# Kernel optimization log

Hardware: AMD Instinct MI355X
Metric: run time of the kernel (lower is better)

## Reference

```python
import jax, jax.numpy as jnp
import numpy as np

N = 8192      # num nodes
E = 262144    # num edges (avg degree 32)
IN = 512
HID = 512
LAT = 128


def setup_inputs() -> dict:
    key = jax.random.key(0)
    ks = jax.random.split(key, 8)
    edge_index = jax.random.randint(ks[0], (2, E), 0, N, dtype=jnp.int64 if jax.config.read('jax_enable_x64') else jnp.int32)
    x = jax.random.normal(ks[1], (N, IN), jnp.float32)
    def w(k, i, o):
        return jax.random.normal(k, (i, o), jnp.float32) * (1.0 / np.sqrt(i))
    return {
        'edge_index': edge_index,
        'x': x,
        'W1': w(ks[2], IN, HID), 'b1': jnp.zeros((HID,), jnp.float32),
        'Wmu': w(ks[3], HID, LAT), 'bmu': jnp.zeros((LAT,), jnp.float32),
        'Wlv': w(ks[4], HID, LAT), 'blv': jnp.zeros((LAT,), jnp.float32),
    }


def gcn_conv(x, row, col, W, b):
    # PyG GCNConv: h = x W; symmetric norm with self-loops (added by caller);
    # out[i] = sum_{(j->i)} d_j^{-1/2} d_i^{-1/2} h[j] + b
    h = x @ W
    ones = jnp.ones((row.shape[0],), h.dtype)
    deg = jax.ops.segment_sum(ones, col, num_segments=N)  # in-degree incl. self-loop
    dinv_sqrt = jnp.where(deg > 0, jax.lax.rsqrt(jnp.maximum(deg, 1e-12)), 0.0)
    norm = dinv_sqrt[row] * dinv_sqrt[col]                # [E+N]
    out = jax.ops.segment_sum(norm[:, None] * h[row], col, num_segments=N)
    return out + b


def reference(edge_index, x, W1, b1, Wmu, bmu, Wlv, blv):
    # add self-loops once, reuse for all layers
    loops = jnp.arange(N, dtype=edge_index.dtype)
    row = jnp.concatenate([edge_index[0], loops])
    col = jnp.concatenate([edge_index[1], loops])

    h = jax.nn.relu(gcn_conv(x, row, col, W1, b1))
    mu = gcn_conv(h, row, col, Wmu, bmu)
    logvar = gcn_conv(h, row, col, Wlv, blv)
    z = mu  # eval-mode reparameterize (deterministic)
    A_pred = jax.nn.sigmoid(z @ z.T)  # [N, N] dot-product decode
    return (A_pred, mu, logvar, z)
```

## Files before the change

kernel.cpp:

```cpp
#include <hip/hip_runtime.h>
#include <math.h>

#define NNODES 8192
#define NEDGES 262144
#define FIN 512
#define FHID 512
#define FLAT 128

typedef unsigned short bfu;
typedef __attribute__((ext_vector_type(8))) short short8;
typedef __attribute__((ext_vector_type(4))) float f32x4;
typedef __attribute__((ext_vector_type(2))) float f32x2;
typedef __attribute__((ext_vector_type(4))) unsigned short us4;

__device__ __forceinline__ float bf2f(unsigned short u) {
    union { unsigned int i; float f; } c; c.i = ((unsigned int)u) << 16; return c.f;
}
__device__ __forceinline__ unsigned short f2bf(float f) {
    union { float f; unsigned int i; } c; c.f = f;
    unsigned int i = c.i;
    unsigned int r = (i + 0x7FFFu + ((i >> 16) & 1u)) >> 16;
    return (unsigned short)r;
}

__global__ void k_zero(int* p, int n) {
    int i = blockIdx.x * blockDim.x + threadIdx.x;
    if (i < n) p[i] = 0;
}

__global__ void k_count(const int* __restrict__ ei, int* __restrict__ deg) {
    int e = blockIdx.x * blockDim.x + threadIdx.x;
    if (e < NEDGES) atomicAdd(&deg[ei[NEDGES + e]], 1);
}

__global__ void k_scan(const int* __restrict__ deg, int* __restrict__ row_start,
                       float* __restrict__ dinv) {
    __shared__ int part[256];
    int t = threadIdx.x, base = t * 32;
    int s = 0;
    for (int i = 0; i < 32; i++) s += deg[base + i];
    part[t] = s;
    __syncthreads();
    for (int off = 1; off < 256; off <<= 1) {
        int v = (t >= off) ? part[t - off] : 0;
        __syncthreads();
        part[t] += v;
        __syncthreads();
    }
    int run = (t == 0) ? 0 : part[t - 1];
    for (int i = 0; i < 32; i++) {
        int d = deg[base + i];
        row_start[base + i] = run;
        run += d;
        dinv[base + i] = rsqrtf((float)(d + 1));
    }
    if (t == 255) row_start[NNODES] = run;
}

__global__ void k_scatter(const int* __restrict__ ei, const int* __restrict__ row_start,
                          int* __restrict__ cursor, int* __restrict__ csr,
                          const float* __restrict__ dinv, float* __restrict__ wcsr) {
    int e = blockIdx.x * blockDim.x + threadIdx.x;
    if (e < NEDGES) {
        int src = ei[e];
        int dst = ei[NEDGES + e];
        int p = atomicAdd(&cursor[dst], 1);
        int pos = row_start[dst] + p;
        csr[pos] = src;
        wcsr[pos] = dinv[src];
    }
}

__global__ void k_prep_const(const float* __restrict__ W1, const float* __restrict__ Wmu,
                             const float* __restrict__ Wlv, const float* __restrict__ x,
                             bfu* __restrict__ Bt1, bfu* __restrict__ Bt2,
                             bfu* __restrict__ xb) {
    __shared__ bfu tile[32][33];
    int b = blockIdx.x;
    if (b < 256) {
        int tx = threadIdx.x & 31, ty = threadIdx.x >> 5;
        int nb = b & 15, kb = b >> 4;
        int n0 = nb * 32, k0 = kb * 32;
#pragma unroll
        for (int i = 0; i < 32; i += 8)
            tile[ty + i][tx] = f2bf(W1[(size_t)(k0 + ty + i) * 512 + n0 + tx]);
        __syncthreads();
#pragma unroll
        for (int i = 0; i < 32; i += 8)
            Bt1[(size_t)(n0 + ty + i) * 512 + k0 + tx] = tile[tx][ty + i];
    } else if (b < 384) {
        int bb = b - 256;
        int tx = threadIdx.x & 31, ty = threadIdx.x >> 5;
        int nb = bb & 7, kb = bb >> 3;
        int n0 = nb * 32, k0 = kb * 32;
        const float* Wsel = (n0 < 128) ? Wmu : Wlv;
        int noff = (n0 < 128) ? 0 : 128;
#pragma unroll
        for (int i = 0; i < 32; i += 8)
            tile[ty + i][tx] = f2bf(Wsel[(size_t)(k0 + ty + i) * 128 + (n0 + tx - noff)]);
        __syncthreads();
#pragma unroll
        for (int i = 0; i < 32; i += 8)
            Bt2[(size_t)(n0 + ty + i) * 512 + k0 + tx] = tile[tx][ty + i];
    } else {
        int i = (b - 384) * 256 + threadIdx.x;
        const float4 v = ((const float4*)x)[i];
        ushort2 lo = {f2bf(v.x), f2bf(v.y)};
        ushort2 hi = {f2bf(v.z), f2bf(v.w)};
        ((ushort2*)xb)[2 * i] = lo;
        ((ushort2*)xb)[2 * i + 1] = hi;
    }
}

template <int TM, int TN>
__global__ void k_gemm_nt(const bfu* __restrict__ A, const bfu* __restrict__ Bt,
                          bfu* __restrict__ C, int M, int N, int K) {
    int wid  = (blockIdx.x * blockDim.x + threadIdx.x) >> 6;
    int lane = threadIdx.x & 63;
    int l = lane & 15, q = lane >> 4;
    int tn = N / (16 * TN);
    int m0 = (wid / tn) * (16 * TM), n0 = (wid % tn) * (16 * TN);

    f32x4 acc[TM][TN];
#pragma unroll
    for (int a = 0; a < TM; a++)
#pragma unroll
        for (int b = 0; b < TN; b++) acc[a][b] = (f32x4){0.f, 0.f, 0.f, 0.f};

    const bfu* Ap = A + (size_t)(m0 + l) * K + q * 8;
    const bfu* Bp = Bt + (size_t)(n0 + l) * K + q * 8;

    for (int k0 = 0; k0 < K; k0 += 32) {
        short8 av[TM], bv[TN];
#pragma unroll
        for (int mi = 0; mi < TM; mi++)
            av[mi] = *(const short8*)(Ap + (size_t)mi * 16 * K + k0);
#pragma unroll
        for (int ni = 0; ni < TN; ni++)
            bv[ni] = *(const short8*)(Bp + (size_t)ni * 16 * K + k0);
#pragma unroll
        for (int mi = 0; mi < TM; mi++)
#pragma unroll
            for (int ni = 0; ni < TN; ni++)
                acc[mi][ni] = __builtin_amdgcn_mfma_f32_16x16x32_bf16(bv[ni], av[mi],
                                                                     acc[mi][ni], 0, 0, 0);
    }

#pragma unroll
    for (int mi = 0; mi < TM; mi++) {
        int row = m0 + mi * 16 + l;
#pragma unroll
        for (int ni = 0; ni < TN; ni++) {
            int col = n0 + ni * 16 + q * 4;
            f32x4 v = acc[mi][ni];
            us4 o = {f2bf(v[0]), f2bf(v[1]), f2bf(v[2]), f2bf(v[3])};
            *(us4*)(C + (size_t)row * N + col) = o;
        }
    }
}

__global__ __launch_bounds__(256) void k_decode_sym(const bfu* __restrict__ Z,
                                                    float* __restrict__ C) {
    __shared__ float ldsT[4][2][16][68];
    int wid  = (blockIdx.x * blockDim.x + threadIdx.x) >> 6;
    int wv   = threadIdx.x >> 6;
    int lane = threadIdx.x & 63;
    int l = lane & 15, q = lane >> 4;

    int idx = wid;
    int ti = (int)((257.0 - sqrt(66049.0 - 8.0 * (double)idx)) * 0.5);
    if (ti > 127) ti = 127;
    if (ti < 0) ti = 0;
    while (ti > 0 && (ti * (257 - ti)) / 2 > idx) ti--;
    while (ti < 127 && ((ti + 1) * (256 - ti)) / 2 <= idx) ti++;
    int tj = ti + (idx - (ti * (257 - ti)) / 2);
    int m0 = ti * 64, n0 = tj * 64;

    f32x4 acc[4][4];
#pragma unroll
    for (int a = 0; a < 4; a++)
#pragma unroll
        for (int b = 0; b < 4; b++) acc[a][b] = (f32x4){0.f, 0.f, 0.f, 0.f};

    const bfu* Ap = Z + (size_t)(m0 + l) * 128 + q * 8;
    const bfu* Bp = Z + (size_t)(n0 + l) * 128 + q * 8;

#pragma unroll
    for (int k0 = 0; k0 < 128; k0 += 32) {
        short8 av[4], bv[4];
#pragma unroll
        for (int mi = 0; mi < 4; mi++)
            av[mi] = *(const short8*)(Ap + (size_t)mi * 16 * 128 + k0);
#pragma unroll
        for (int ni = 0; ni < 4; ni++)
            bv[ni] = *(const short8*)(Bp + (size_t)ni * 16 * 128 + k0);
#pragma unroll
        for (int mi = 0; mi < 4; mi++)
#pragma unroll
            for (int ni = 0; ni < 4; ni++)
                acc[mi][ni] = __builtin_amdgcn_mfma_f32_16x16x32_bf16(bv[ni], av[mi],
                                                                     acc[mi][ni], 0, 0, 0);
    }

#pragma unroll
    for (int mi = 0; mi < 4; mi++)
#pragma unroll
        for (int ni = 0; ni < 4; ni++)
#pragma unroll
            for (int r = 0; r < 4; r++)
                acc[mi][ni][r] = __builtin_amdgcn_rcpf(1.0f + __expf(-acc[mi][ni][r]));

#pragma unroll
    for (int mi = 0; mi < 4; mi++) {
        int row = m0 + mi * 16 + l;
#pragma unroll
        for (int ni = 0; ni < 4; ni++) {
            int col = n0 + ni * 16 + q * 4;
            __builtin_nontemporal_store(acc[mi][ni], (f32x4*)(C + (size_t)row * 8192 + col));
        }
    }

    if (ti != tj) {
#pragma unroll
        for (int ni = 0; ni < 4; ni++) {
            int p = ni & 1;
#pragma unroll
            for (int mi = 0; mi < 4; mi++)
#pragma unroll
                for (int r = 0; r < 4; r++)
                    ldsT[wv][p][q * 4 + r][mi * 16 + l] = acc[mi][ni][r];
            asm volatile("s_waitcnt lgkmcnt(0)" ::: "memory");
#pragma unroll
            for (int j = 0; j < 16; j++) {
                float v = ldsT[wv][p][j][lane];
                __builtin_nontemporal_store(
                    v, C + (size_t)(n0 + ni * 16 + j) * 8192 + m0 + lane);
            }
        }
    }
}

template <int F>
__device__ __forceinline__ void agg_core(const bfu* __restrict__ hin,
                                         const int* __restrict__ csr,
                                         const float* __restrict__ wcsr,
                                         int s, int e, int i, int f, float di,
                                         float& a0, float& a1) {
    a0 = 0.f; a1 = 0.f;
    int ed = s;
    for (; ed + 4 <= e; ed += 4) {
        int s0 = csr[ed], s1 = csr[ed + 1], s2 = csr[ed + 2], s3 = csr[ed + 3];
        float w0 = wcsr[ed], w1 = wcsr[ed + 1], w2 = wcsr[ed + 2], w3 = wcsr[ed + 3];
        unsigned int p0 = *(const unsigned int*)(hin + (size_t)s0 * F + f);
        unsigned int p1 = *(const unsigned int*)(hin + (size_t)s1 * F + f);
        unsigned int p2 = *(const unsigned int*)(hin + (size_t)s2 * F + f);
        unsigned int p3 = *(const unsigned int*)(hin + (size_t)s3 * F + f);
        a0 += w0 * bf2f((unsigned short)(p0 & 0xFFFF));
        a1 += w0 * bf2f((unsigned short)(p0 >> 16));
        a0 += w1 * bf2f((unsigned short)(p1 & 0xFFFF));
        a1 += w1 * bf2f((unsigned short)(p1 >> 16));
        a0 += w2 * bf2f((unsigned short)(p2 & 0xFFFF));
        a1 += w2 * bf2f((unsigned short)(p2 >> 16));
        a0 += w3 * bf2f((unsigned short)(p3 & 0xFFFF));
        a1 += w3 * bf2f((unsigned short)(p3 >> 16));
    }
    for (; ed < e; ed++) {
        int src = csr[ed];
        float w = wcsr[ed];
        unsigned int pk = *(const unsigned int*)(hin + (size_t)src * F + f);
        a0 += w * bf2f((unsigned short)(pk & 0xFFFF));
        a1 += w * bf2f((unsigned short)(pk >> 16));
    }
    unsigned int pk = *(const unsigned int*)(hin + (size_t)i * F + f);
    a0 += di * bf2f((unsigned short)(pk & 0xFFFF));
    a1 += di * bf2f((unsigned short)(pk >> 16));
}

__global__ void k_agg1(const bfu* __restrict__ hin, const int* __restrict__ csr,
                       const float* __restrict__ wcsr, const int* __restrict__ rs,
                       const float* __restrict__ dinv, const float* __restrict__ bias,
                       bfu* __restrict__ hout) {
    int i = blockIdx.x;
    int f = threadIdx.x * 2;
    float di = dinv[i];
    float a0, a1;
    agg_core<FHID>(hin, csr, wcsr, rs[i], rs[i + 1], i, f, di, a0, a1);
    float o0 = fmaxf(di * a0 + bias[f], 0.f);
    float o1 = fmaxf(di * a1 + bias[f + 1], 0.f);
    unsigned int outw = (unsigned int)f2bf(o0) | ((unsigned int)f2bf(o1) << 16);
    *(unsigned int*)(hout + (size_t)i * FHID + f) = outw;
}

__global__ void k_agg2(const bfu* __restrict__ hin, const int* __restrict__ csr,
                       const float* __restrict__ wcsr, const int* __restrict__ rs,
                       const float* __restrict__ dinv, const float* __restrict__ bmu,
                       const float* __restrict__ blv, float* __restrict__ out_mu,
                       float* __restrict__ out_lv, float* __restrict__ out_z,
                       bfu* __restrict__ ws_z) {
    int i = blockIdx.x;
    int f = threadIdx.x * 2;
    float di = dinv[i];
    float a0, a1;
    agg_core<256>(hin, csr, wcsr, rs[i], rs[i + 1], i, f, di, a0, a1);
    float v0 = di * a0, v1 = di * a1;
    if (f < 128) {
        v0 += bmu[f]; v1 += bmu[f + 1];
        f32x2 fv = {v0, v1};
        __builtin_nontemporal_store(fv, (f32x2*)(out_mu + (size_t)i * FLAT + f));
        __builtin_nontemporal_store(fv, (f32x2*)(out_z + (size_t)i * FLAT + f));
        unsigned int bw = (unsigned int)f2bf(v0) | ((unsigned int)f2bf(v1) << 16);
        *(unsigned int*)(ws_z + (size_t)i * FLAT + f) = bw;
    } else {
        int fl = f - 128;
        v0 += blv[fl]; v1 += blv[fl + 1];
        f32x2 fv = {v0, v1};
        __builtin_nontemporal_store(fv, (f32x2*)(out_lv + (size_t)i * FLAT + fl));
    }
}

extern "C" void kernel_launch(void* const* d_in, const int* in_sizes, int n_in,
                              void* d_out, int out_size, void* d_ws, size_t ws_size,
                              hipStream_t stream) {
    const int*   ei  = (const int*)d_in[0];
    const float* x   = (const float*)d_in[1];
    const float* W1  = (const float*)d_in[2];
    const float* b1  = (const float*)d_in[3];
    const float* Wmu = (const float*)d_in[4];
    const float* bmu = (const float*)d_in[5];
    const float* Wlv = (const float*)d_in[6];
    const float* blv = (const float*)d_in[7];
    float* out = (float*)d_out;

    char* wsb = (char*)d_ws;
    size_t off = 0;
    auto alloc = [&](size_t bytes) -> char* {
        char* p = wsb + off;
        off += (bytes + 255) & ~(size_t)255;
        return p;
    };
    int*   deg       = (int*)alloc(NNODES * 4);
    int*   cursor    = (int*)alloc(NNODES * 4);
    int*   row_start = (int*)alloc((NNODES + 1) * 4);
    float* dinv      = (float*)alloc(NNODES * 4);
    int*   csr       = (int*)alloc(NEDGES * 4);
    float* wcsr      = (float*)alloc(NEDGES * 4);
    bfu*   Bt1       = (bfu*)alloc(512 * 512 * 2);
    bfu*   Bt2       = (bfu*)alloc(256 * 512 * 2);
    bfu*   xb        = (bfu*)alloc((size_t)NNODES * FIN * 2);
    bfu*   h0        = (bfu*)alloc((size_t)NNODES * FHID * 2);
    bfu*   h         = (bfu*)alloc((size_t)NNODES * FHID * 2);
    bfu*   hml       = (bfu*)alloc((size_t)NNODES * 256 * 2);
    bfu*   zb        = (bfu*)alloc((size_t)NNODES * FLAT * 2);

    float* out_mu = out + (size_t)NNODES * NNODES;
    float* out_lv = out_mu + (size_t)NNODES * FLAT;
    float* out_z  = out_lv + (size_t)NNODES * FLAT;

    k_zero<<<(2 * NNODES + 255) / 256, 256, 0, stream>>>(deg, 2 * NNODES);
    k_count<<<NEDGES / 256, 256, 0, stream>>>(ei, deg);
    k_scan<<<1, 256, 0, stream>>>(deg, row_start, dinv);
    k_scatter<<<NEDGES / 256, 256, 0, stream>>>(ei, row_start, cursor, csr, dinv, wcsr);
    k_prep_const<<<256 + 128 + 4096, 256, 0, stream>>>(W1, Wmu, Wlv, x, Bt1, Bt2, xb);

    k_gemm_nt<4, 2><<<(8192 / 64) * (512 / 32) / 4, 256, 0, stream>>>(
        xb, Bt1, h0, 8192, 512, 512);
    k_agg1<<<NNODES, 256, 0, stream>>>(h0, csr, wcsr, row_start, dinv, b1, h);

    k_gemm_nt<2, 2><<<(8192 / 32) * (256 / 32) / 4, 256, 0, stream>>>(
        h, Bt2, hml, 8192, 256, 512);
    k_agg2<<<NNODES, 128, 0, stream>>>(hml, csr, wcsr, row_start, dinv, bmu, blv,
                                       out_mu, out_lv, out_z, zb);

    k_decode_sym<<<8256 / 4, 256, 0, stream>>>(zb, out);
}
```

Before: 450.9 us.

## Vectorize GCN aggregation per wavefront, pack edge pairs, merge prep kernels

Aggregation kernels now assign one wavefront per node, and each lane loads 8 (or 4) bf16 features as a single wide vector. Neighbour index and weight are packed into one int2 array so each edge needs a single load. The CSR scatter is merged with the weight/x preparation kernel to save a launch. The decode transpose store now writes 16-byte vectors instead of scalars. Together these aim to cut memory instruction count and launch overhead, at the cost of more registers per lane and fewer independent edges in flight per lane.

Measured after the change: 448.6 us. About the same (-0.5%).

```diff
diff --git a/kernel.cpp b/kernel.cpp
--- a/kernel.cpp
+++ b/kernel.cpp
@@ -21,6 +21,23 @@
     unsigned int i = c.i;
     unsigned int r = (i + 0x7FFFu + ((i >> 16) & 1u)) >> 16;
     return (unsigned short)r;
+}
+
+__device__ __forceinline__ void acc8(float* acc, uint4 v, float w) {
+    acc[0] += w * bf2f((unsigned short)(v.x & 0xFFFF));
+    acc[1] += w * bf2f((unsigned short)(v.x >> 16));
+    acc[2] += w * bf2f((unsigned short)(v.y & 0xFFFF));
+    acc[3] += w * bf2f((unsigned short)(v.y >> 16));
+    acc[4] += w * bf2f((unsigned short)(v.z & 0xFFFF));
+    acc[5] += w * bf2f((unsigned short)(v.z >> 16));
+    acc[6] += w * bf2f((unsigned short)(v.w & 0xFFFF));
+    acc[7] += w * bf2f((unsigned short)(v.w >> 16));
+}
+__device__ __forceinline__ void acc4(float* acc, uint2 v, float w) {
+    acc[0] += w * bf2f((unsigned short)(v.x & 0xFFFF));
+    acc[1] += w * bf2f((unsigned short)(v.x >> 16));
+    acc[2] += w * bf2f((unsigned short)(v.y & 0xFFFF));
+    acc[3] += w * bf2f((unsigned short)(v.y >> 16));
 }
 
 __global__ void k_zero(int* p, int n) {
@@ -57,29 +74,28 @@
     if (t == 255) row_start[NNODES] = run;
 }
 
-__global__ void k_scatter(const int* __restrict__ ei, const int* __restrict__ row_start,
-                          int* __restrict__ cursor, int* __restrict__ csr,
-                          const float* __restrict__ dinv, float* __restrict__ wcsr) {
-    int e = blockIdx.x * blockDim.x + threadIdx.x;
-    if (e < NEDGES) {
+__global__ void k_scatter_prep(const int* __restrict__ ei, const int* __restrict__ row_start,
+                               int* __restrict__ cursor, int2* __restrict__ ep,
+                               const float* __restrict__ dinv,
+                               const float* __restrict__ W1, const float* __restrict__ Wmu,
+                               const float* __restrict__ Wlv, const float* __restrict__ x,
+                               bfu* __restrict__ Bt1, bfu* __restrict__ Bt2,
+                               bfu* __restrict__ xb) {
+    __shared__ bfu tile[32][33];
+    int b = blockIdx.x;
+    if (b < 1024) {
+        int e = b * 256 + threadIdx.x;
         int src = ei[e];
         int dst = ei[NEDGES + e];
         int p = atomicAdd(&cursor[dst], 1);
-        int pos = row_start[dst] + p;
-        csr[pos] = src;
-        wcsr[pos] = dinv[src];
-    }
-}
-
-__global__ void k_prep_const(const float* __restrict__ W1, const float* __restrict__ Wmu,
-                             const float* __restrict__ Wlv, const float* __restrict__ x,
-                             bfu* __restrict__ Bt1, bfu* __restrict__ Bt2,
-                             bfu* __restrict__ xb) {
-    __shared__ bfu tile[32][33];
-    int b = blockIdx.x;
-    if (b < 256) {
+        int2 pr;
+        pr.x = src;
+        pr.y = __float_as_int(dinv[src]);
+        ep[row_start[dst] + p] = pr;
+    } else if (b < 1280) {
+        int bb = b - 1024;
         int tx = threadIdx.x & 31, ty = threadIdx.x >> 5;
-        int nb = b & 15, kb = b >> 4;
+        int nb = bb & 15, kb = bb >> 4;
         int n0 = nb * 32, k0 = kb * 32;
 #pragma unroll
         for (int i = 0; i < 32; i += 8)
@@ -88,8 +104,8 @@
 #pragma unroll
         for (int i = 0; i < 32; i += 8)
             Bt1[(size_t)(n0 + ty + i) * 512 + k0 + tx] = tile[tx][ty + i];
-    } else if (b < 384) {
-        int bb = b - 256;
+    } else if (b < 1408) {
+        int bb = b - 1280;
         int tx = threadIdx.x & 31, ty = threadIdx.x >> 5;
         int nb = bb & 7, kb = bb >> 3;
         int n0 = nb * 32, k0 = kb * 32;
@@ -103,7 +119,7 @@
         for (int i = 0; i < 32; i += 8)
             Bt2[(size_t)(n0 + ty + i) * 512 + k0 + tx] = tile[tx][ty + i];
     } else {
-        int i = (b - 384) * 256 + threadIdx.x;
+        int i = (b - 1408) * 256 + threadIdx.x;
         const float4 v = ((const float4*)x)[i];
         ushort2 lo = {f2bf(v.x), f2bf(v.y)};
         ushort2 hi = {f2bf(v.z), f2bf(v.w)};
@@ -231,90 +247,112 @@
                     ldsT[wv][p][q * 4 + r][mi * 16 + l] = acc[mi][ni][r];
             asm volatile("s_waitcnt lgkmcnt(0)" ::: "memory");
 #pragma unroll
-            for (int j = 0; j < 16; j++) {
-                float v = ldsT[wv][p][j][lane];
+            for (int jj = 0; jj < 4; jj++) {
+                f32x4 v = *(const f32x4*)&ldsT[wv][p][jj * 4 + q][l * 4];
                 __builtin_nontemporal_store(
-                    v, C + (size_t)(n0 + ni * 16 + j) * 8192 + m0 + lane);
+                    v, (f32x4*)(C + (size_t)(n0 + ni * 16 + jj * 4 + q) * 8192 + m0 + l * 4));
             }
         }
     }
 }
 
-template <int F>
-__device__ __forceinline__ void agg_core(const bfu* __restrict__ hin,
-                                         const int* __restrict__ csr,
-                                         const float* __restrict__ wcsr,
-                                         int s, int e, int i, int f, float di,
-                                         float& a0, float& a1) {
-    a0 = 0.f; a1 = 0.f;
+__global__ void k_agg1(const bfu* __restrict__ hin, const int2* __restrict__ ep,
+                       const int* __restrict__ rs, const float* __restrict__ dinv,
+                       const float* __restrict__ bias, bfu* __restrict__ hout) {
+    int node = blockIdx.x * 4 + (threadIdx.x >> 6);
+    int lane = threadIdx.x & 63;
+    int f = lane * 8;
+    int s = rs[node], e = rs[node + 1];
+    float di = dinv[node];
+    float acc[8];
+#pragma unroll
+    for (int k = 0; k < 8; k++) acc[k] = 0.f;
+    const bfu* hf = hin + f;
+
     int ed = s;
-    for (; ed + 4 <= e; ed += 4) {
-        int s0 = csr[ed], s1 = csr[ed + 1], s2 = csr[ed + 2], s3 = csr[ed + 3];
-        float w0 = wcsr[ed], w1 = wcsr[ed + 1], w2 = wcsr[ed + 2], w3 = wcsr[ed + 3];
-        unsigned int p0 = *(const unsigned int*)(hin + (size_t)s0 * F + f);
-        unsigned int p1 = *(const unsigned int*)(hin + (size_t)s1 * F + f);
-        unsigned int p2 = *(const unsigned int*)(hin + (size_t)s2 * F + f);
-        unsigned int p3 = *(const unsigned int*)(hin + (size_t)s3 * F + f);
-        a0 += w0 * bf2f((unsigned short)(p0 & 0xFFFF));
-        a1 += w0 * bf2f((unsigned short)(p0 >> 16));
-        a0 += w1 * bf2f((unsigned short)(p1 & 0xFFFF));
-        a1 += w1 * bf2f((unsigned short)(p1 >> 16));
-        a0 += w2 * bf2f((unsigned short)(p2 & 0xFFFF));
-        a1 += w2 * bf2f((unsigned short)(p2 >> 16));
-        a0 += w3 * bf2f((unsigned short)(p3 & 0xFFFF));
-        a1 += w3 * bf2f((unsigned short)(p3 >> 16));
-    }
-    for (; ed < e; ed++) {
-        int src = csr[ed];
-        float w = wcsr[ed];
-        unsigned int pk = *(const unsigned int*)(hin + (size_t)src * F + f);
-        a0 += w * bf2f((unsigned short)(pk & 0xFFFF));
-        a1 += w * bf2f((unsigned short)(pk >> 16));
-    }
-    unsigned int pk = *(const unsigned int*)(hin + (size_t)i * F + f);
-    a0 += di * bf2f((unsigned short)(pk & 0xFFFF));
-    a1 += di * bf2f((unsigned short)(pk >> 16));
-}
-
-__global__ void k_agg1(const bfu* __restrict__ hin, const int* __restrict__ csr,
-                       const float* __restrict__ wcsr, const int* __restrict__ rs,
-                       const float* __restrict__ dinv, const float* __restrict__ bias,
-                       bfu* __restrict__ hout) {
-    int i = blockIdx.x;
-    int f = threadIdx.x * 2;
-    float di = dinv[i];
-    float a0, a1;
-    agg_core<FHID>(hin, csr, wcsr, rs[i], rs[i + 1], i, f, di, a0, a1);
-    float o0 = fmaxf(di * a0 + bias[f], 0.f);
-    float o1 = fmaxf(di * a1 + bias[f + 1], 0.f);
-    unsigned int outw = (unsigned int)f2bf(o0) | ((unsigned int)f2bf(o1) << 16);
-    *(unsigned int*)(hout + (size_t)i * FHID + f) = outw;
-}
-
-__global__ void k_agg2(const bfu* __restrict__ hin, const int* __restrict__ csr,
-                       const float* __restrict__ wcsr, const int* __restrict__ rs,
-                       const float* __restrict__ dinv, const float* __restrict__ bmu,
-                       const float* __restrict__ blv, float* __restrict__ out_mu,
-                       float* __restrict__ out_lv, float* __restrict__ out_z,
-                       bfu* __restrict__ ws_z) {
-    int i = blockIdx.x;
-    int f = threadIdx.x * 2;
-    float di = dinv[i];
-    float a0, a1;
-    agg_core<256>(hin, csr, wcsr, rs[i], rs[i + 1], i, f, di, a0, a1);
-    float v0 = di * a0, v1 = di * a1;
+    for (; ed + 2 <= e; ed += 2) {
+        int2 p0 = ep[ed], p1 = ep[ed + 1];
+        uint4 v0 = *(const uint4*)(hf + (size_t)p0.x * FHID);
+        uint4 v1 = *(const uint4*)(hf + (size_t)p1.x * FHID);
+        acc8(acc, v0, __int_as_float(p0.y));
+        acc8(acc, v1, __int_as_float(p1.y));
+    }
+    if (ed < e) {
+        int2 p0 = ep[ed];
+        uint4 v0 = *(const uint4*)(hf + (size_t)p0.x * FHID);
+        acc8(acc, v0, __int_as_float(p0.y));
+    }
+    {
+        uint4 vs = *(const uint4*)(hf + (size_t)node * FHID);
+        acc8(acc, vs, di);
+    }
+
+    f32x4 b0 = *(const f32x4*)(bias + f);
+    f32x4 b1v = *(const f32x4*)(bias + f + 4);
+    float o[8];
+#pragma unroll
+    for (int k = 0; k < 4; k++) o[k] = fmaxf(di * acc[k] + b0[k], 0.f);
+#pragma unroll
+    for (int k = 0; k < 4; k++) o[4 + k] = fmaxf(di * acc[4 + k] + b1v[k], 0.f);
+    uint4 ow;
+    ow.x = (unsigned int)f2bf(o[0]) | ((unsigned int)f2bf(o[1]) << 16);
+    ow.y = (unsigned int)f2bf(o[2]) | ((unsigned int)f2bf(o[3]) << 16);
+    ow.z = (unsigned int)f2bf(o[4]) | ((unsigned int)f2bf(o[5]) << 16);
+    ow.w = (unsigned int)f2bf(o[6]) | ((unsigned int)f2bf(o[7]) << 16);
+    *(uint4*)(hout + (size_t)node * FHID + f) = ow;
+}
+
+__global__ void k_agg2(const bfu* __restrict__ hin, const int2* __restrict__ ep,
+                       const int* __restrict__ rs, const float* __restrict__ dinv,
+                       const float* __restrict__ bmu, const float* __restrict__ blv,
+                       float* __restrict__ out_mu, float* __restrict__ out_lv,
+                       float* __restrict__ out_z, bfu* __restrict__ ws_z) {
+    int node = blockIdx.x * 4 + (threadIdx.x >> 6);
+    int lane = threadIdx.x & 63;
+    int f = lane * 4;
+    int s = rs[node], e = rs[node + 1];
+    float di = dinv[node];
+    float acc[4];
+#pragma unroll
+    for (int k = 0; k < 4; k++) acc[k] = 0.f;
+    const bfu* hf = hin + f;
+
+    int ed = s;
+    for (; ed + 2 <= e; ed += 2) {
+        int2 p0 = ep[ed], p1 = ep[ed + 1];
+        uint2 v0 = *(const uint2*)(hf + (size_t)p0.x * 256);
+        uint2 v1 = *(const uint2*)(hf + (size_t)p1.x * 256);
+        acc4(acc, v0, __int_as_float(p0.y));
+        acc4(acc, v1, __int_as_float(p1.y));
+    }
+    if (ed < e) {
+        int2 p0 = ep[ed];
+        uint2 v0 = *(const uint2*)(hf + (size_t)p0.x * 256);
+        acc4(acc, v0, __int_as_float(p0.y));
+    }
+    {
+        uint2 vs = *(const uint2*)(hf + (size_t)node * 256);
+        acc4(acc, vs, di);
+    }
+
     if (f < 128) {
-        v0 += bmu[f]; v1 += bmu[f + 1];
-        f32x2 fv = {v0, v1};
-        __builtin_nontemporal_store(fv, (f32x2*)(out_mu + (size_t)i * FLAT + f));
-        __builtin_nontemporal_store(fv, (f32x2*)(out_z + (size_t)i * FLAT + f));
-        unsigned int bw = (unsigned int)f2bf(v0) | ((unsigned int)f2bf(v1) << 16);
-        *(unsigned int*)(ws_z + (size_t)i * FLAT + f) = bw;
+        f32x4 bm = *(const f32x4*)(bmu + f);
+        f32x4 fv;
+#pragma unroll
+        for (int k = 0; k < 4; k++) fv[k] = di * acc[k] + bm[k];
+        __builtin_nontemporal_store(fv, (f32x4*)(out_mu + (size_t)node * FLAT + f));
+        __builtin_nontemporal_store(fv, (f32x4*)(out_z + (size_t)node * FLAT + f));
+        uint2 bw;
+        bw.x = (unsigned int)f2bf(fv[0]) | ((unsigned int)f2bf(fv[1]) << 16);
+        bw.y = (unsigned int)f2bf(fv[2]) | ((unsigned int)f2bf(fv[3]) << 16);
+        *(uint2*)(ws_z + (size_t)node * FLAT + f) = bw;
     } else {
         int fl = f - 128;
-        v0 += blv[fl]; v1 += blv[fl + 1];
-        f32x2 fv = {v0, v1};
-        __builtin_nontemporal_store(fv, (f32x2*)(out_lv + (size_t)i * FLAT + fl));
+        f32x4 bl = *(const f32x4*)(blv + fl);
+        f32x4 fv;
+#pragma unroll
+        for (int k = 0; k < 4; k++) fv[k] = di * acc[k] + bl[k];
+        __builtin_nontemporal_store(fv, (f32x4*)(out_lv + (size_t)node * FLAT + fl));
     }
 }
 
@@ -342,8 +380,7 @@
     int*   cursor    = (int*)alloc(NNODES * 4);
     int*   row_start = (int*)alloc((NNODES + 1) * 4);
     float* dinv      = (float*)alloc(NNODES * 4);
-    int*   csr       = (int*)alloc(NEDGES * 4);
-    float* wcsr      = (float*)alloc(NEDGES * 4);
+    int2*  ep        = (int2*)alloc((size_t)NEDGES * 8);
     bfu*   Bt1       = (bfu*)alloc(512 * 512 * 2);
     bfu*   Bt2       = (bfu*)alloc(256 * 512 * 2);
     bfu*   xb        = (bfu*)alloc((size_t)NNODES * FIN * 2);
@@ -359,17 +396,17 @@
     k_zero<<<(2 * NNODES + 255) / 256, 256, 0, stream>>>(deg, 2 * NNODES);
     k_count<<<NEDGES / 256, 256, 0, stream>>>(ei, deg);
     k_scan<<<1, 256, 0, stream>>>(deg, row_start, dinv);
-    k_scatter<<<NEDGES / 256, 256, 0, stream>>>(ei, row_start, cursor, csr, dinv, wcsr);
-    k_prep_const<<<256 + 128 + 4096, 256, 0, stream>>>(W1, Wmu, Wlv, x, Bt1, Bt2, xb);
+    k_scatter_prep<<<1024 + 256 + 128 + 4096, 256, 0, stream>>>(
+        ei, row_start, cursor, ep, dinv, W1, Wmu, Wlv, x, Bt1, Bt2, xb);
 
     k_gemm_nt<4, 2><<<(8192 / 64) * (512 / 32) / 4, 256, 0, stream>>>(
         xb, Bt1, h0, 8192, 512, 512);
-    k_agg1<<<NNODES, 256, 0, stream>>>(h0, csr, wcsr, row_start, dinv, b1, h);
+    k_agg1<<<NNODES / 4, 256, 0, stream>>>(h0, ep, row_start, dinv, b1, h);
 
     k_gemm_nt<2, 2><<<(8192 / 32) * (256 / 32) / 4, 256, 0, stream>>>(
         h, Bt2, hml, 8192, 256, 512);
-    k_agg2<<<NNODES, 128, 0, stream>>>(hml, csr, wcsr, row_start, dinv, bmu, blv,
-                                       out_mu, out_lv, out_z, zb);
+    k_agg2<<<NNODES / 4, 256, 0, stream>>>(hml, ep, row_start, dinv, bmu, blv,
+                                           out_mu, out_lv, out_z, zb);
 
     k_decode_sym<<<8256 / 4, 256, 0, stream>>>(zb, out);
 }
```
